# Kernel optimization log

Measured on AMD Instinct MI355X. Metric: run time of the kernel, lower is better.

The kernel has to match this reference:

```python
import jax, jax.numpy as jnp
import numpy as np

IN_FEATURES = 1024
OUT_FEATURES = 1024
KNOT_COUNT = 5
ORDER = 3
BATCH = 4096


def setup_inputs() -> dict:
    key = jax.random.key(0)
    k1, k2 = jax.random.split(key)
    x = jax.random.normal(k1, (BATCH, IN_FEATURES), dtype=jnp.float32)
    knots = jnp.linspace(-1.0, 1.0, KNOT_COUNT, dtype=jnp.float32)
    coeffs = jax.random.normal(k2, (KNOT_COUNT + ORDER, OUT_FEATURES, IN_FEATURES), dtype=jnp.float32)
    return {"x": x, "knots": knots, "coeffs": coeffs}


def _bspline_bases(x, knots, order):
    # x: [B, I]; knots: [K] uniform grid. Extend to K + 2*order + 1 knots so
    # the number of degree-`order` basis functions is K + order.
    h = knots[1] - knots[0]
    left = knots[0] + h * jnp.arange(-order, 0, dtype=knots.dtype)
    right = knots[-1] + h * jnp.arange(1, order + 2, dtype=knots.dtype)
    t = jnp.concatenate([left, knots, right])  # [K + 2*order + 1]
    xe = x[..., None]  # [B, I, 1]
    # degree-0 indicator bases: [B, I, m-1]
    bases = ((xe >= t[:-1]) & (xe < t[1:])).astype(x.dtype)
    # Cox-de Boor recursion up to degree `order` (vectorized over batch/features)
    for k in range(1, order + 1):
        left_num = (xe - t[: -(k + 1)]) / (t[k:-1] - t[: -(k + 1)])
        right_num = (t[k + 1:] - xe) / (t[k + 1:] - t[1:-k])
        bases = left_num * bases[..., :-1] + right_num * bases[..., 1:]
    return bases  # [B, I, K + order]


def reference(x, knots, coeffs):
    # Faithful fused version of the per-(i,j) python loops:
    # spline_j(b) = sum_n B_n(x[b,i]) * coeffs[n, j, i]; output sums over i.
    bases = _bspline_bases(x, knots, ORDER)          # [B, I, N]
    return jnp.einsum('bin,noi->bo', bases, coeffs)  # [B, O]
```

## Files before the change

kernel.cpp:

```cpp
#include <hip/hip_runtime.h>
#include <hip/hip_bf16.h>
#include <cstdint>
#include <cstddef>

#define IN_F   1024
#define OUT_F  1024
#define NB     8
#define BATCH  4096
#define KTOT   (NB * IN_F)

typedef __attribute__((ext_vector_type(4)))  float  f32x4;
typedef __attribute__((ext_vector_type(8)))  float  f32x8;
typedef __attribute__((ext_vector_type(8)))  __bf16 bf16x8;
typedef __attribute__((ext_vector_type(4)))  unsigned short u16x4;

#define GLDS16(g, l)                                                     \
    __builtin_amdgcn_global_load_lds(                                    \
        (const __attribute__((address_space(1))) void*)(g),              \
        (__attribute__((address_space(3))) void*)(l), 16, 0, 0)

__device__ __forceinline__ void spline_w(float r, float w[4]) {
    const float r2 = r * r, r3 = r2 * r;
    const float omr = 1.0f - r;
    w[0] = omr * omr * omr * (1.0f / 6.0f);
    w[1] = (3.0f * r3 - 6.0f * r2 + 4.0f) * (1.0f / 6.0f);
    w[2] = (-3.0f * r3 + 3.0f * r2 + 3.0f * r + 1.0f) * (1.0f / 6.0f);
    w[3] = r3 * (1.0f / 6.0f);
}

__global__ void k_prep(const float* __restrict__ coeffs, __bf16* __restrict__ Wb,
                       const float* __restrict__ x, __bf16* __restrict__ A) {
    const int bb = blockIdx.x;
    if (bb < 4096) {
        const size_t g   = (size_t)bb * blockDim.x + threadIdx.x;
        const size_t idx = g * 8;
        const int i = (int)(idx & 1023);
        const int o = (int)((idx >> 10) & 1023);
        const int c = (i >> 3) & 7;
        const int isw = (i & ~63) | ((c ^ (o & 7)) << 3);
        f32x8 v = *(const f32x8*)(coeffs + idx);
        bf16x8 ov = __builtin_convertvector(v, bf16x8);
        *(bf16x8*)(Wb + (idx - i) + isw) = ov;
    } else {
        const int g    = (bb - 4096) * blockDim.x + threadIdx.x;
        const int flat = g * 4;
        const int b = flat >> 10, i = flat & 1023;
        f32x4 xv = *(const f32x4*)(x + flat);

        float w[4][4];
        int   jj[4];
#pragma unroll
        for (int e = 0; e < 4; ++e) {
            const float u  = (xv[e] + 2.5f) * 2.0f;
            const float jf = floorf(u);
            jj[e] = (int)jf;
            spline_w(u - jf, w[e]);
        }

        const int c   = (i >> 3) & 7;
        const int isw = (i & ~63) | ((c ^ (b & 7)) << 3) | (i & 7);
        __bf16* base = A + (size_t)b * KTOT + isw;
#pragma unroll
        for (int n = 0; n < NB; ++n) {
            u16x4 pack;
#pragma unroll
            for (int e = 0; e < 4; ++e) {
                const int d = n - jj[e] + 3;
                float v = (d == 0) ? w[e][0]
                        : (d == 1) ? w[e][1]
                        : (d == 2) ? w[e][2]
                        : (d == 3) ? w[e][3] : 0.0f;
                __bf16 h = (__bf16)v;
                pack[e] = __builtin_bit_cast(unsigned short, h);
            }
            *(u16x4*)(base + n * IN_F) = pack;
        }
    }
}

#define BM 256
#define BN 128
#define BK 64
#define NT (KTOT / BK)
#define SPLITK 2
#define NTS (NT / SPLITK)
#define BUFSZ 49152

__global__ __launch_bounds__(512) void k_gemm(const __bf16* __restrict__ A,
                                              const __bf16* __restrict__ W,
                                              float* __restrict__ C,
                                              float* __restrict__ P) {
    __shared__ __align__(16) char ls[3 * BUFSZ];

    const int fid = blockIdx.x;
    const int xcd = fid & 7;
    const int s   = fid >> 3;
    const int y   = xcd + 8 * (s & 1);
    const int xb  = (s >> 1) & 7;
    const int kz  = s >> 4;

    const int o0   = xb * BN;
    const int b0   = y * BM;
    const int tid  = threadIdx.x;
    const int lane = tid & 63;
    const int wv   = tid >> 6;
    const int wr   = wv >> 1;
    const int wc   = wv & 1;
    const int l15  = lane & 15;
    const int lhi  = lane >> 4;

    f32x4 acc[4][4] = {};

    const int srow  = tid >> 3;
    const int scol8 = (tid & 7) * 8;

    auto STAGE_A = [&](int buf, int kt) {
        const int k0 = kt * BK;
        char* la = ls + buf * BUFSZ;
#pragma unroll
        for (int it = 0; it < 4; ++it) {
            const __bf16* ga = A + (size_t)(b0 + srow + it * 64) * KTOT + k0 + scol8;
            GLDS16(ga, la + tid * 16 + it * 8192);
        }
    };
    auto STAGE_B = [&](int buf, int kt) {
        const int k0 = kt * BK;
        const int n  = k0 >> 10;
        const int i0 = k0 & 1023;
        char* lb = ls + buf * BUFSZ + 32768;
#pragma unroll
        for (int it = 0; it < 2; ++it) {
            const __bf16* gw = W + ((size_t)n << 20)
                                 + (size_t)(o0 + srow + it * 64) * IN_F + i0 + scol8;
            GLDS16(gw, lb + tid * 16 + it * 8192);
        }
    };

    const int ktBeg = kz * NTS;
    STAGE_A(0, ktBeg);     STAGE_B(0, ktBeg);
    STAGE_A(1, ktBeg + 1); STAGE_B(1, ktBeg + 1);

    int cur = 0, nxt = 2;
    for (int t = 0; t < NTS; ++t) {
        if (t < NTS - 1) asm volatile("s_waitcnt vmcnt(6)" ::: "memory");
        else             asm volatile("s_waitcnt vmcnt(0)" ::: "memory");
        __builtin_amdgcn_s_barrier();
        __builtin_amdgcn_sched_barrier(0);

        const char* la = ls + cur * BUFSZ;
        const char* lb = la + 32768;
        const bool doStage = (t + 2 < NTS);
        const int  kt2     = ktBeg + t + 2;

        {
            bf16x8 af[4], bfr[4];
#pragma unroll
            for (int m = 0; m < 4; ++m) {
                const int r = wr * 64 + m * 16 + l15;
                const int c = lhi ^ (r & 7);
                af[m] = *(const bf16x8*)(la + r * 128 + c * 16);
            }
#pragma unroll
            for (int nn = 0; nn < 4; ++nn) {
                const int r = wc * 64 + nn * 16 + l15;
                const int c = lhi ^ (r & 7);
                bfr[nn] = *(const bf16x8*)(lb + r * 128 + c * 16);
            }
            if (doStage) STAGE_A(nxt, kt2);
            __builtin_amdgcn_s_barrier();
            __builtin_amdgcn_s_setprio(1);
#pragma unroll
            for (int m = 0; m < 4; ++m)
#pragma unroll
                for (int nn = 0; nn < 4; ++nn)
                    acc[m][nn] = __builtin_amdgcn_mfma_f32_16x16x32_bf16(
                        af[m], bfr[nn], acc[m][nn], 0, 0, 0);
            __builtin_amdgcn_s_setprio(0);
            __builtin_amdgcn_s_barrier();
        }
        {
            bf16x8 af[4], bfr[4];
#pragma unroll
            for (int m = 0; m < 4; ++m) {
                const int r = wr * 64 + m * 16 + l15;
                const int c = (4 + lhi) ^ (r & 7);
                af[m] = *(const bf16x8*)(la + r * 128 + c * 16);
            }
#pragma unroll
            for (int nn = 0; nn < 4; ++nn) {
                const int r = wc * 64 + nn * 16 + l15;
                const int c = (4 + lhi) ^ (r & 7);
                bfr[nn] = *(const bf16x8*)(lb + r * 128 + c * 16);
            }
            if (doStage) STAGE_B(nxt, kt2);
            __builtin_amdgcn_s_barrier();
            __builtin_amdgcn_s_setprio(1);
#pragma unroll
            for (int m = 0; m < 4; ++m)
#pragma unroll
                for (int nn = 0; nn < 4; ++nn)
                    acc[m][nn] = __builtin_amdgcn_mfma_f32_16x16x32_bf16(
                        af[m], bfr[nn], acc[m][nn], 0, 0, 0);
            __builtin_amdgcn_s_setprio(0);
        }
        cur = (cur == 2) ? 0 : cur + 1;
        nxt = (nxt == 2) ? 0 : nxt + 1;
    }

    float* dst = (kz == 0) ? C : P;
    const int crow = lhi * 4;
#pragma unroll
    for (int m = 0; m < 4; ++m) {
#pragma unroll
        for (int nn = 0; nn < 4; ++nn) {
            float* cp = dst + (size_t)(b0 + wr * 64 + m * 16 + crow) * OUT_F
                            + o0 + wc * 64 + nn * 16 + l15;
#pragma unroll
            for (int j = 0; j < 4; ++j)
                cp[(size_t)j * OUT_F] = acc[m][nn][j];
        }
    }
}

__global__ void k_add(float* __restrict__ C, const float* __restrict__ P) {
    const size_t g = (size_t)(blockIdx.x * blockDim.x + threadIdx.x) * 4;
    f32x4 a = *(const f32x4*)(C + g);
    f32x4 b = *(const f32x4*)(P + g);
    a += b;
    *(f32x4*)(C + g) = a;
}

__global__ void k_naive(const float* __restrict__ x, const float* __restrict__ coeffs,
                        float* __restrict__ out) {
    const int b = blockIdx.y * 16 + (threadIdx.x >> 4);
    const int o = blockIdx.x * 16 + (threadIdx.x & 15);
    float sum = 0.0f;
    for (int i = 0; i < IN_F; ++i) {
        const float u  = (x[(size_t)b * IN_F + i] + 2.5f) * 2.0f;
        const float jf = floorf(u);
        const int   j  = (int)jf;
        float w[4];
        spline_w(u - jf, w);
#pragma unroll
        for (int m = 0; m < 4; ++m) {
            const int idx = j - 3 + m;
            if (idx >= 0 && idx < NB)
                sum += w[m] * coeffs[(size_t)idx * OUT_F * IN_F + (size_t)o * IN_F + i];
        }
    }
    out[(size_t)b * OUT_F + o] = sum;
}

extern "C" void kernel_launch(void* const* d_in, const int* in_sizes, int n_in,
                              void* d_out, int out_size, void* d_ws, size_t ws_size,
                              hipStream_t stream) {
    const float* x      = (const float*)d_in[0];
    const float* coeffs = (const float*)d_in[2];
    float* out = (float*)d_out;

    const size_t needA = (size_t)BATCH * KTOT * sizeof(__bf16);
    const size_t needW = (size_t)NB * OUT_F * IN_F * sizeof(__bf16);
    const size_t needP = (size_t)BATCH * OUT_F * sizeof(float);

    if (ws_size >= needA + needW + needP) {
        __bf16* A  = (__bf16*)d_ws;
        __bf16* Wb = (__bf16*)((char*)d_ws + needA);
        float*  P  = (float*)((char*)d_ws + needA + needW);

        hipLaunchKernelGGL(k_prep, dim3(8192), dim3(256), 0, stream,
                           coeffs, Wb, x, A);
        hipLaunchKernelGGL(k_gemm, dim3(256), dim3(512), 0, stream, A, Wb, out, P);
        hipLaunchKernelGGL(k_add, dim3(BATCH * OUT_F / 4 / 256), dim3(256), 0,
                           stream, out, P);
    } else {
        hipLaunchKernelGGL(k_naive, dim3(OUT_F / 16, BATCH / 16), dim3(256), 0,
                           stream, x, coeffs, out);
    }
}
```

Baseline: 120.6 us.

## Use 256x256 tiles with 4-way split-K and quadrant-interleaved double-buffered pipeline

Grows the GEMM block tile from 256x128 to 256x256 with 8 waves laid out 2x4. Each K-tile is split into four MFMA quadrants, and half-tile global-to-LDS stages are interleaved between them over a two-buffer ring instead of three. Split-K rises to 4 when workspace allows, with a reduction kernel summing three partial buffers, so the grid stays at 256 blocks. The larger tile improves operand reuse, at the cost of more accumulator registers, extra partial-sum memory traffic, and many more barriers.

```diff
diff --git a/kernel.cpp b/kernel.cpp
--- a/kernel.cpp
+++ b/kernel.cpp
@@ -78,155 +78,180 @@
     }
 }
 
-#define BM 256
-#define BN 128
 #define BK 64
-#define NT (KTOT / BK)
-#define SPLITK 2
-#define NTS (NT / SPLITK)
-#define BUFSZ 49152
-
+
+#define BAR1()  do { __builtin_amdgcn_sched_barrier(0);                    \
+                     __builtin_amdgcn_s_barrier();                         \
+                     asm volatile("s_waitcnt lgkmcnt(0)" ::: "memory");    \
+                     __builtin_amdgcn_sched_barrier(0); } while (0)
+#define BAR2()  do { __builtin_amdgcn_sched_barrier(0);                    \
+                     __builtin_amdgcn_s_barrier(); } while (0)
+
+#define QUAD(mh, nh, aa, bb)                                               \
+    do {                                                                   \
+        __builtin_amdgcn_s_setprio(1);                                     \
+        _Pragma("unroll")                                                  \
+        for (int m = 0; m < 4; ++m)                                        \
+            _Pragma("unroll")                                              \
+            for (int n2 = 0; n2 < 2; ++n2)                                 \
+                _Pragma("unroll")                                          \
+                for (int k = 0; k < 2; ++k)                                \
+                    acc[(mh)*4+m][(nh)*2+n2] =                             \
+                        __builtin_amdgcn_mfma_f32_16x16x32_bf16(           \
+                            aa[m][k], bb[n2][k], acc[(mh)*4+m][(nh)*2+n2], \
+                            0, 0, 0);                                      \
+        __builtin_amdgcn_s_setprio(0);                                     \
+    } while (0)
+
+template <int SK>
 __global__ __launch_bounds__(512) void k_gemm(const __bf16* __restrict__ A,
                                               const __bf16* __restrict__ W,
                                               float* __restrict__ C,
                                               float* __restrict__ P) {
-    __shared__ __align__(16) char ls[3 * BUFSZ];
+    constexpr int NKT = 128 / SK;
+    constexpr int NIT = NKT / 2;
+    __shared__ __align__(16) char ls[2][65536];
 
     const int fid = blockIdx.x;
-    const int xcd = fid & 7;
     const int s   = fid >> 3;
-    const int y   = xcd + 8 * (s & 1);
-    const int xb  = (s >> 1) & 7;
-    const int kz  = s >> 4;
-
-    const int o0   = xb * BN;
-    const int b0   = y * BM;
+    const int row = (fid & 7) * 2 + (s & 1);
+    const int col = (s >> 1) & 3;
+    const int kz  = s >> 3;
+
+    const int b0   = row * 256;
+    const int o0   = col * 256;
     const int tid  = threadIdx.x;
     const int lane = tid & 63;
     const int wv   = tid >> 6;
-    const int wr   = wv >> 1;
-    const int wc   = wv & 1;
+    const int wr   = wv >> 2;
+    const int wc   = wv & 3;
     const int l15  = lane & 15;
     const int lhi  = lane >> 4;
 
-    f32x4 acc[4][4] = {};
+    f32x4 acc[8][4] = {};
 
     const int srow  = tid >> 3;
     const int scol8 = (tid & 7) * 8;
 
-    auto STAGE_A = [&](int buf, int kt) {
+    auto stA = [&](int db, int kt, int h) {
         const int k0 = kt * BK;
-        char* la = ls + buf * BUFSZ;
-#pragma unroll
-        for (int it = 0; it < 4; ++it) {
-            const __bf16* ga = A + (size_t)(b0 + srow + it * 64) * KTOT + k0 + scol8;
-            GLDS16(ga, la + tid * 16 + it * 8192);
+        char* la = ls[db];
+#pragma unroll
+        for (int j = 0; j < 2; ++j) {
+            const int it = 2 * h + j;
+            GLDS16(A + (size_t)(b0 + srow + it * 64) * KTOT + k0 + scol8,
+                   la + tid * 16 + it * 8192);
         }
     };
-    auto STAGE_B = [&](int buf, int kt) {
+    auto stB = [&](int db, int kt, int h) {
         const int k0 = kt * BK;
         const int n  = k0 >> 10;
         const int i0 = k0 & 1023;
-        char* lb = ls + buf * BUFSZ + 32768;
-#pragma unroll
-        for (int it = 0; it < 2; ++it) {
-            const __bf16* gw = W + ((size_t)n << 20)
-                                 + (size_t)(o0 + srow + it * 64) * IN_F + i0 + scol8;
-            GLDS16(gw, lb + tid * 16 + it * 8192);
+        char* lb = ls[db] + 32768;
+#pragma unroll
+        for (int j = 0; j < 2; ++j) {
+            const int it = 2 * h + j;
+            GLDS16(W + ((size_t)n << 20)
+                     + (size_t)(o0 + srow + it * 64) * IN_F + i0 + scol8,
+                   lb + tid * 16 + it * 8192);
         }
     };
-
-    const int ktBeg = kz * NTS;
-    STAGE_A(0, ktBeg);     STAGE_B(0, ktBeg);
-    STAGE_A(1, ktBeg + 1); STAGE_B(1, ktBeg + 1);
-
-    int cur = 0, nxt = 2;
-    for (int t = 0; t < NTS; ++t) {
-        if (t < NTS - 1) asm volatile("s_waitcnt vmcnt(6)" ::: "memory");
-        else             asm volatile("s_waitcnt vmcnt(0)" ::: "memory");
-        __builtin_amdgcn_s_barrier();
-        __builtin_amdgcn_sched_barrier(0);
-
-        const char* la = ls + cur * BUFSZ;
-        const char* lb = la + 32768;
-        const bool doStage = (t + 2 < NTS);
-        const int  kt2     = ktBeg + t + 2;
-
-        {
-            bf16x8 af[4], bfr[4];
-#pragma unroll
-            for (int m = 0; m < 4; ++m) {
-                const int r = wr * 64 + m * 16 + l15;
-                const int c = lhi ^ (r & 7);
-                af[m] = *(const bf16x8*)(la + r * 128 + c * 16);
+    auto rdA = [&](const char* la, int mh, bf16x8 aa[4][2]) {
+#pragma unroll
+        for (int m = 0; m < 4; ++m)
+#pragma unroll
+            for (int k = 0; k < 2; ++k) {
+                const int r = wr * 64 + mh * 128 + m * 16 + l15;
+                const int c = (k * 4 + lhi) ^ (r & 7);
+                aa[m][k] = *(const bf16x8*)(la + r * 128 + c * 16);
             }
-#pragma unroll
-            for (int nn = 0; nn < 4; ++nn) {
-                const int r = wc * 64 + nn * 16 + l15;
-                const int c = lhi ^ (r & 7);
-                bfr[nn] = *(const bf16x8*)(lb + r * 128 + c * 16);
+    };
+    auto rdB = [&](const char* lb, int nh, bf16x8 bb[2][2]) {
+#pragma unroll
+        for (int n2 = 0; n2 < 2; ++n2)
+#pragma unroll
+            for (int k = 0; k < 2; ++k) {
+                const int r = wc * 32 + nh * 128 + n2 * 16 + l15;
+                const int c = (k * 4 + lhi) ^ (r & 7);
+                bb[n2][k] = *(const bf16x8*)(lb + r * 128 + c * 16);
             }
-            if (doStage) STAGE_A(nxt, kt2);
-            __builtin_amdgcn_s_barrier();
-            __builtin_amdgcn_s_setprio(1);
-#pragma unroll
-            for (int m = 0; m < 4; ++m)
-#pragma unroll
-                for (int nn = 0; nn < 4; ++nn)
-                    acc[m][nn] = __builtin_amdgcn_mfma_f32_16x16x32_bf16(
-                        af[m], bfr[nn], acc[m][nn], 0, 0, 0);
-            __builtin_amdgcn_s_setprio(0);
-            __builtin_amdgcn_s_barrier();
-        }
-        {
-            bf16x8 af[4], bfr[4];
-#pragma unroll
-            for (int m = 0; m < 4; ++m) {
-                const int r = wr * 64 + m * 16 + l15;
-                const int c = (4 + lhi) ^ (r & 7);
-                af[m] = *(const bf16x8*)(la + r * 128 + c * 16);
-            }
-#pragma unroll
-            for (int nn = 0; nn < 4; ++nn) {
-                const int r = wc * 64 + nn * 16 + l15;
-                const int c = (4 + lhi) ^ (r & 7);
-                bfr[nn] = *(const bf16x8*)(lb + r * 128 + c * 16);
-            }
-            if (doStage) STAGE_B(nxt, kt2);
-            __builtin_amdgcn_s_barrier();
-            __builtin_amdgcn_s_setprio(1);
-#pragma unroll
-            for (int m = 0; m < 4; ++m)
-#pragma unroll
-                for (int nn = 0; nn < 4; ++nn)
-                    acc[m][nn] = __builtin_amdgcn_mfma_f32_16x16x32_bf16(
-                        af[m], bfr[nn], acc[m][nn], 0, 0, 0);
-            __builtin_amdgcn_s_setprio(0);
-        }
-        cur = (cur == 2) ? 0 : cur + 1;
-        nxt = (nxt == 2) ? 0 : nxt + 1;
+    };
+
+    const int ktBeg = kz * NKT;
+
+    stA(0, ktBeg, 0); stB(0, ktBeg, 0); stB(0, ktBeg, 1); stA(0, ktBeg, 1);
+    stA(1, ktBeg + 1, 0); stB(1, ktBeg + 1, 0); stB(1, ktBeg + 1, 1);
+    asm volatile("s_waitcnt vmcnt(6)" ::: "memory");
+    __builtin_amdgcn_sched_barrier(0);
+    __builtin_amdgcn_s_barrier();
+
+    const char* la0 = ls[0]; const char* lb0 = ls[0] + 32768;
+    const char* la1 = ls[1]; const char* lb1 = ls[1] + 32768;
+    bf16x8 a[4][2], br0[2][2], br1[2][2];
+
+    for (int i8 = 0; i8 < NIT; ++i8) {
+        const int t0 = ktBeg + 2 * i8;
+        const bool s2 = (2 * i8 + 2 < NKT), s3 = (2 * i8 + 3 < NKT);
+
+        rdA(la0, 0, a); rdB(lb0, 0, br0);
+        stA(1, t0 + 1, 1);
+        BAR1(); QUAD(0, 0, a, br0); BAR2();
+        rdB(lb0, 1, br1);
+        if (s2) stA(0, t0 + 2, 0);
+        BAR1(); QUAD(0, 1, a, br1); BAR2();
+        rdA(la0, 1, a);
+        if (s2) stB(0, t0 + 2, 0);
+        BAR1(); QUAD(1, 1, a, br1); BAR2();
+        if (s2) {
+            stB(0, t0 + 2, 1);
+            asm volatile("s_waitcnt vmcnt(6)" ::: "memory");
+        } else {
+            asm volatile("s_waitcnt vmcnt(0)" ::: "memory");
+        }
+        BAR1(); QUAD(1, 0, a, br0); BAR2();
+        rdA(la1, 0, a); rdB(lb1, 0, br0);
+        if (s2) stA(0, t0 + 2, 1);
+        BAR1(); QUAD(0, 0, a, br0); BAR2();
+        rdB(lb1, 1, br1);
+        if (s3) stA(1, t0 + 3, 0);
+        BAR1(); QUAD(0, 1, a, br1); BAR2();
+        rdA(la1, 1, a);
+        if (s3) stB(1, t0 + 3, 0);
+        BAR1(); QUAD(1, 1, a, br1); BAR2();
+        if (s3) {
+            stB(1, t0 + 3, 1);
+            asm volatile("s_waitcnt vmcnt(6)" ::: "memory");
+        } else {
+            asm volatile("s_waitcnt vmcnt(0)" ::: "memory");
+        }
+        BAR1(); QUAD(1, 0, a, br0); BAR2();
     }
 
-    float* dst = (kz == 0) ? C : P;
-    const int crow = lhi * 4;
-#pragma unroll
-    for (int m = 0; m < 4; ++m) {
-#pragma unroll
-        for (int nn = 0; nn < 4; ++nn) {
-            float* cp = dst + (size_t)(b0 + wr * 64 + m * 16 + crow) * OUT_F
-                            + o0 + wc * 64 + nn * 16 + l15;
-#pragma unroll
-            for (int j = 0; j < 4; ++j)
-                cp[(size_t)j * OUT_F] = acc[m][nn][j];
-        }
-    }
-}
-
+    float* dst = (kz == 0) ? C : P + (size_t)(kz - 1) * BATCH * OUT_F;
+#pragma unroll
+    for (int mh = 0; mh < 2; ++mh)
+#pragma unroll
+        for (int m = 0; m < 4; ++m)
+#pragma unroll
+            for (int nh = 0; nh < 2; ++nh)
+#pragma unroll
+                for (int n2 = 0; n2 < 2; ++n2) {
+                    float* cp = dst
+                        + (size_t)(b0 + wr * 64 + mh * 128 + m * 16 + lhi * 4) * OUT_F
+                        + o0 + wc * 32 + nh * 128 + n2 * 16 + l15;
+#pragma unroll
+                    for (int j = 0; j < 4; ++j)
+                        cp[(size_t)j * OUT_F] = acc[mh * 4 + m][nh * 2 + n2][j];
+                }
+}
+
+template <int NP>
 __global__ void k_add(float* __restrict__ C, const float* __restrict__ P) {
     const size_t g = (size_t)(blockIdx.x * blockDim.x + threadIdx.x) * 4;
     f32x4 a = *(const f32x4*)(C + g);
-    f32x4 b = *(const f32x4*)(P + g);
-    a += b;
+#pragma unroll
+    for (int p = 0; p < NP; ++p)
+        a += *(const f32x4*)(P + (size_t)p * BATCH * OUT_F + g);
     *(f32x4*)(C + g) = a;
 }
 
@@ -260,18 +285,26 @@
 
     const size_t needA = (size_t)BATCH * KTOT * sizeof(__bf16);
     const size_t needW = (size_t)NB * OUT_F * IN_F * sizeof(__bf16);
-    const size_t needP = (size_t)BATCH * OUT_F * sizeof(float);
-
-    if (ws_size >= needA + needW + needP) {
+    const size_t oneP  = (size_t)BATCH * OUT_F * sizeof(float);
+
+    if (ws_size >= needA + needW + oneP) {
         __bf16* A  = (__bf16*)d_ws;
         __bf16* Wb = (__bf16*)((char*)d_ws + needA);
         float*  P  = (float*)((char*)d_ws + needA + needW);
 
         hipLaunchKernelGGL(k_prep, dim3(8192), dim3(256), 0, stream,
                            coeffs, Wb, x, A);
-        hipLaunchKernelGGL(k_gemm, dim3(256), dim3(512), 0, stream, A, Wb, out, P);
-        hipLaunchKernelGGL(k_add, dim3(BATCH * OUT_F / 4 / 256), dim3(256), 0,
-                           stream, out, P);
+        if (ws_size >= needA + needW + 3 * oneP) {
+            hipLaunchKernelGGL(k_gemm<4>, dim3(256), dim3(512), 0, stream,
+                               A, Wb, out, P);
+            hipLaunchKernelGGL(k_add<3>, dim3(BATCH * OUT_F / 4 / 256), dim3(256),
+                               0, stream, out, P);
+        } else {
+            hipLaunchKernelGGL(k_gemm<2>, dim3(128), dim3(512), 0, stream,
+                               A, Wb, out, P);
+            hipLaunchKernelGGL(k_add<1>, dim3(BATCH * OUT_F / 4 / 256), dim3(256),
+                               0, stream, out, P);
+        }
     } else {
         hipLaunchKernelGGL(k_naive, dim3(OUT_F / 16, BATCH / 16), dim3(256), 0,
                            stream, x, coeffs, out);
```

New measurement: 121.5 us. About the same (+0.8%).
